# Optimization experiments

Measured on AMD Instinct MI355X. Metric: run time of the kernel, lower is better.

The kernel has to match this reference:

```python
import jax, jax.numpy as jnp
import numpy as np

PHI_C = 0.9
ALPHA = 0.9
EPS = 1e-06
K_MAX = 100


def setup_inputs() -> dict:
    key = jax.random.key(0)
    k1, k2, k3 = jax.random.split(key, 3)
    B, D_IN, D_H, D_OUT = 16384, 1024, 4096, 1024
    x = jax.random.normal(k1, (B, D_IN), dtype=jnp.float32)
    W1 = jax.random.normal(k2, (D_IN, D_H), dtype=jnp.float32) * 0.02
    b1 = jnp.zeros((D_H,), dtype=jnp.float32)
    W2 = jax.random.normal(k3, (D_H, D_OUT), dtype=jnp.float32) * 0.02
    b2 = jnp.zeros((D_OUT,), dtype=jnp.float32)
    return {"x": x, "W1": W1, "b1": b1, "W2": W2, "b2": b2}


def _base_net(x, W1, b1, W2, b2):
    h = jax.nn.relu(x @ W1 + b1)
    return h @ W2 + b2  # [B, D_OUT]


def _fixed_point(out):
    # y_{k+1} = y_k + alpha * phi_c * tanh(out - y_k), with early exit when
    # max|y_{k+1} - y_k| < eps (the converging step IS applied, as in torch).
    y0 = jnp.zeros_like(out)

    def step(carry, _):
        y, done = carry
        y_next = y + ALPHA * PHI_C * jnp.tanh(out - y)
        converged = jnp.max(jnp.abs(y_next - y)) < EPS
        y_new = jnp.where(done, y, y_next)
        return (y_new, done | converged), None

    (y, _), _ = jax.lax.scan(step, (y0, jnp.array(False)), None, length=K_MAX)
    return y


def reference(x, W1, b1, W2, b2):
    out = _base_net(x, W1, b1, W2, b2)
    return _fixed_point(out)
```

## Files before the change

kernel.cpp:

```cpp
#include <hip/hip_runtime.h>
#include <hip/hip_bf16.h>
#include <stdint.h>


#define DEV __device__ __forceinline__

typedef short bf16x8 __attribute__((ext_vector_type(8)));
typedef float f32x16 __attribute__((ext_vector_type(16)));

typedef __attribute__((address_space(1))) const unsigned char* gptr1_t;
typedef __attribute__((address_space(3))) unsigned char* lptr3_t;

DEV void async_copy16(const void* g, void* l) {
  __builtin_amdgcn_global_load_lds((gptr1_t)g, (lptr3_t)l, 16, 0, 0);
}

DEV unsigned short f2bf(float f) {
  union { float f; unsigned u; } v; v.f = f;
  unsigned u = v.u + 0x7FFFu + ((v.u >> 16) & 1u);
  return (unsigned short)(u >> 16);
}

#define BAR()    __builtin_amdgcn_s_barrier()
#define VMW(n)   asm volatile("s_waitcnt vmcnt(" #n ")" ::: "memory")
#define SCHEDB() __builtin_amdgcn_sched_barrier(0)


__global__ void cvt_f32_bf16(const float4* __restrict__ in,
                             ushort4* __restrict__ out, int n4) {
  int i = blockIdx.x * blockDim.x + threadIdx.x;
  if (i >= n4) return;
  float4 v = in[i];
  ushort4 o;
  o.x = f2bf(v.x); o.y = f2bf(v.y); o.z = f2bf(v.z); o.w = f2bf(v.w);
  out[i] = o;
}

__global__ void transpose_f32_bf16(const float* __restrict__ in,
                                   unsigned short* __restrict__ out,
                                   int R, int C) {
  __shared__ float tile[32][33];
  int c0 = blockIdx.x * 32, r0 = blockIdx.y * 32;
  int tx = threadIdx.x, ty = threadIdx.y;
#pragma unroll
  for (int i = 0; i < 32; i += 8)
    tile[ty + i][tx] = in[(long)(r0 + ty + i) * C + (c0 + tx)];
  __syncthreads();
#pragma unroll
  for (int i = 0; i < 32; i += 8)
    out[(long)(c0 + ty + i) * R + (r0 + tx)] = f2bf(tile[tx][ty + i]);
}


#define LDA(base, m, ks) \
  (*(const bf16x8*)((base) + abase + (m) * 4096 + (c0 ^ ((ks) << 5))))
#define LDB(base, n, ks) \
  (*(const bf16x8*)((base) + bbase + (n) * 4096 + (c0 ^ ((ks) << 5))))

#define COMPUTE(aB, bB)                                                       \
  _Pragma("unroll") for (int ks = 0; ks < 4; ++ks) {                          \
    bf16x8 af[4], bfr[4];                                                     \
    _Pragma("unroll") for (int i = 0; i < 4; ++i) {                           \
      af[i] = LDA(aB, i, ks);                                                 \
      bfr[i] = LDB(bB, i, ks);                                                \
    }                                                                         \
    _Pragma("unroll") for (int m_ = 0; m_ < 4; ++m_)                          \
    _Pragma("unroll") for (int n_ = 0; n_ < 4; ++n_)                          \
      acc[m_][n_] = __builtin_amdgcn_mfma_f32_32x32x16_bf16(                  \
          af[m_], bfr[n_], acc[m_][n_], 0, 0, 0);                             \
  }

#define STAGE(buf_, koff_)                                                    \
  _Pragma("unroll") for (int j = 0; j < 8; ++j) {                             \
    async_copy16(gAb + (size_t)j * 32 * K + (koff_),                          \
                 ldsAw + (buf_) * 32768 + j * 4096);                          \
    async_copy16(gBb + (size_t)j * 32 * K + (koff_),                          \
                 ldsBw + (buf_) * 32768 + j * 4096);                          \
  }

template <bool RELU_BF16>
__global__ __launch_bounds__(256, 1)
void gemm256(const unsigned short* __restrict__ A,
             const unsigned short* __restrict__ BT,
             const float* __restrict__ bias,
             void* __restrict__ Cout,
             int M, int N, int K, int nbn_shift) {
  extern __shared__ char lds[];
  char* ldsA = lds;
  char* ldsB = lds + 65536;

  const int tid = threadIdx.x;
  const int wave = tid >> 6, lane = tid & 63;
  const int wr = wave >> 1, wc = wave & 1;

  const int nwg = gridDim.x;
  const int wg = blockIdx.x;
  const int swz = (wg & 7) * (nwg >> 3) + (wg >> 3);
  const int bm = swz >> nbn_shift;
  const int bn = swz & ((1 << nbn_shift) - 1);
  const int m0 = bm << 8, n0 = bn << 8;

  const int srow = lane >> 3;
  const int skb = ((lane & 7) ^ srow) << 3;
  const unsigned short* gAb = A + (size_t)(m0 + wave * 8 + srow) * K + skb;
  const unsigned short* gBb = BT + (size_t)(n0 + wave * 8 + srow) * K + skb;
  char* ldsAw = ldsA + wave * 1024;
  char* ldsBw = ldsB + wave * 1024;

  const int cl31 = lane & 31, lg2 = lane >> 5;
  const int c0 = ((lg2 ^ (lane & 7)) << 4);
  const int abase = (wr * 128 + cl31) * 128;
  const int bbase = (wc * 128 + cl31) * 128;

  f32x16 acc[4][4] = {};

  STAGE(0, 0);
  STAGE(1, 64);
  VMW(16);
  BAR();

  const int NT = K >> 6;

  for (int t = 0; t < NT - 2; ++t) {
    const char* aB = ldsA + (t & 1) * 32768;
    const char* bB = ldsB + (t & 1) * 32768;
    COMPUTE(aB, bB);
    BAR();
    SCHEDB();
    STAGE(t & 1, (t + 2) << 6);
    VMW(16);
    BAR();
  }

  COMPUTE(ldsA, ldsB);
  BAR();
  VMW(0);
  BAR();
  COMPUTE((ldsA + 32768), (ldsB + 32768));

  const int ccol = n0 + wc * 128;
  const int crow = m0 + wr * 128;
  float bv[4];
#pragma unroll
  for (int n = 0; n < 4; ++n) bv[n] = bias[ccol + n * 32 + cl31];

  if (RELU_BF16) {
    unsigned short* O = (unsigned short*)Cout;
#pragma unroll
    for (int m = 0; m < 4; ++m)
#pragma unroll
      for (int rr = 0; rr < 4; ++rr)
#pragma unroll
        for (int q = 0; q < 4; ++q) {
          size_t r = (size_t)(crow + m * 32 + lg2 * 4 + q + 8 * rr) * N;
#pragma unroll
          for (int n = 0; n < 4; ++n) {
            float v = acc[m][n][rr * 4 + q] + bv[n];
            O[r + ccol + n * 32 + cl31] = f2bf(fmaxf(v, 0.0f));
          }
        }
  } else {
    float* O = (float*)Cout;
#pragma unroll
    for (int m = 0; m < 4; ++m)
#pragma unroll
      for (int rr = 0; rr < 4; ++rr)
#pragma unroll
        for (int q = 0; q < 4; ++q) {
          size_t r = (size_t)(crow + m * 32 + lg2 * 4 + q + 8 * rr) * N;
#pragma unroll
          for (int n = 0; n < 4; ++n)
            O[r + ccol + n * 32 + cl31] = acc[m][n][rr * 4 + q] + bv[n];
        }
  }
}


extern "C" void kernel_launch(void* const* d_in, const int* in_sizes, int n_in,
                              void* d_out, int out_size, void* d_ws,
                              size_t ws_size, hipStream_t stream) {
  const float* x  = (const float*)d_in[0];
  const float* W1 = (const float*)d_in[1];
  const float* b1 = (const float*)d_in[2];
  const float* W2 = (const float*)d_in[3];
  const float* b2 = (const float*)d_in[4];
  float* out = (float*)d_out;

  const int B = 16384, DIN = 1024, DH = 4096, DOUT = 1024;

  size_t need = (size_t)B * DIN * 2 + (size_t)DIN * DH * 2 +
                (size_t)DH * DOUT * 2 + (size_t)B * DH * 2;
  if (ws_size < need) return;

  char* ws = (char*)d_ws;
  unsigned short* xb  = (unsigned short*)ws;  ws += (size_t)B * DIN * 2;
  unsigned short* w1t = (unsigned short*)ws;  ws += (size_t)DIN * DH * 2;
  unsigned short* w2t = (unsigned short*)ws;  ws += (size_t)DH * DOUT * 2;
  unsigned short* h   = (unsigned short*)ws;

  hipFuncSetAttribute((const void*)gemm256<true>,
                      hipFuncAttributeMaxDynamicSharedMemorySize, 131072);
  hipFuncSetAttribute((const void*)gemm256<false>,
                      hipFuncAttributeMaxDynamicSharedMemorySize, 131072);

  int n4 = B * DIN / 4;
  cvt_f32_bf16<<<n4 / 256, 256, 0, stream>>>((const float4*)x, (ushort4*)xb, n4);
  transpose_f32_bf16<<<dim3(DH / 32, DIN / 32), dim3(32, 8), 0, stream>>>(W1, w1t, DIN, DH);
  transpose_f32_bf16<<<dim3(DOUT / 32, DH / 32), dim3(32, 8), 0, stream>>>(W2, w2t, DH, DOUT);

  gemm256<true><<<dim3((B / 256) * (DH / 256)), 256, 131072, stream>>>(
      xb, w1t, b1, h, B, DH, DIN, 4);
  gemm256<false><<<dim3((B / 256) * (DOUT / 256)), 256, 131072, stream>>>(
      h, w2t, b2, out, B, DOUT, DH, 2);
}
```

Measured before the change: 302.5 us.

## Make first GEMM persistent over four M-tiles and adjust LDS swizzle

The first GEMM now launches one block per CU, and each block walks four consecutive 256-row tiles for a fixed column tile. The double-buffered K pipeline runs continuously across tiles, with the bias/ReLU/bf16 epilogue inserted when each tile finishes. This is meant to remove per-block prologue/drain costs and wave-quantization tail effects. Both GEMMs also gain an extra wave-dependent XOR in the LDS swizzle to reduce bank conflicts. The epilogue stores now stall the pipeline mid-stream, and the grid mapping assumes the fixed problem shape.

After: 429.2 us. 1.42x slower.

```diff
diff --git a/kernel.cpp b/kernel.cpp
--- a/kernel.cpp
+++ b/kernel.cpp
@@ -52,17 +52,17 @@
 }
 
 
-#define LDA(base, m, ks) \
-  (*(const bf16x8*)((base) + abase + (m) * 4096 + (c0 ^ ((ks) << 5))))
-#define LDB(base, n, ks) \
-  (*(const bf16x8*)((base) + bbase + (n) * 4096 + (c0 ^ ((ks) << 5))))
-
-#define COMPUTE(aB, bB)                                                       \
+#define ILDA(base, m, ks) \
+  (*(const bf16x8*)((base) + i_abase + (m) * 4096 + (i_c0 ^ ((ks) << 5))))
+#define ILDB(base, n, ks) \
+  (*(const bf16x8*)((base) + i_bbase + (n) * 4096 + (i_c0 ^ ((ks) << 5))))
+
+#define ICOMPUTE(aB, bB)                                                      \
   _Pragma("unroll") for (int ks = 0; ks < 4; ++ks) {                          \
     bf16x8 af[4], bfr[4];                                                     \
     _Pragma("unroll") for (int i = 0; i < 4; ++i) {                           \
-      af[i] = LDA(aB, i, ks);                                                 \
-      bfr[i] = LDB(bB, i, ks);                                                \
+      af[i] = ILDA(aB, i, ks);                                                \
+      bfr[i] = ILDB(bB, i, ks);                                               \
     }                                                                         \
     _Pragma("unroll") for (int m_ = 0; m_ < 4; ++m_)                          \
     _Pragma("unroll") for (int n_ = 0; n_ < 4; ++n_)                          \
@@ -70,7 +70,103 @@
           af[m_], bfr[n_], acc[m_][n_], 0, 0, 0);                             \
   }
 
-#define STAGE(buf_, koff_)                                                    \
+
+#define PSTAGE(buf_, g_)                                                      \
+  { const int t_ = (g_) & 15;                                                 \
+    const size_t ja_ = (size_t)((g_) >> 4) * ((size_t)K << 8);                \
+    _Pragma("unroll") for (int j = 0; j < 8; ++j) {                           \
+      async_copy16(gAb + ja_ + (size_t)j * 32 * K + (t_ << 6),                \
+                   ldsAw + (buf_) * 32768 + j * 4096);                        \
+      async_copy16(gBb + (size_t)j * 32 * K + (t_ << 6),                      \
+                   ldsBw + (buf_) * 32768 + j * 4096);                        \
+    } }
+
+#define PEPI(j_)                                                              \
+  { const size_t crow = (size_t)m0base + (size_t)(j_) * 256 + wr * 128;       \
+    _Pragma("unroll") for (int m = 0; m < 4; ++m)                             \
+    _Pragma("unroll") for (int rr = 0; rr < 4; ++rr)                          \
+    _Pragma("unroll") for (int q = 0; q < 4; ++q) {                           \
+      size_t r = (crow + m * 32 + lg2 * 4 + q + 8 * rr) * Ndim;               \
+      _Pragma("unroll") for (int n = 0; n < 4; ++n) {                         \
+        float v = acc[m][n][rr * 4 + q] + bv[n];                              \
+        O[r + ccol + n * 32 + cl31] = f2bf(fmaxf(v, 0.0f));                   \
+      } } }
+
+#define ZEROACC()                                                             \
+  _Pragma("unroll") for (int m = 0; m < 4; ++m)                               \
+  _Pragma("unroll") for (int n = 0; n < 4; ++n)                               \
+  _Pragma("unroll") for (int e = 0; e < 16; ++e) acc[m][n][e] = 0.0f;
+
+__global__ __launch_bounds__(256, 1)
+void gemm_ilp4p(const unsigned short* __restrict__ A,
+                const unsigned short* __restrict__ BT,
+                const float* __restrict__ bias,
+                unsigned short* __restrict__ O,
+                int Kd, int Ndim) {
+  extern __shared__ char lds[];
+  char* ldsA = lds;
+  char* ldsB = lds + 65536;
+  const int K = Kd;
+
+  const int tid = threadIdx.x;
+  const int wave = tid >> 6, lane = tid & 63;
+  const int wr = wave >> 1, wc = wave & 1;
+
+  const int nwg = gridDim.x;
+  const int wg = blockIdx.x;
+  const int swz = (wg & 7) * (nwg >> 3) + (wg >> 3);
+  const int bn = swz & 15;
+  const int grp = swz >> 4;
+  const int n0 = bn << 8;
+  const int m0base = grp << 10;
+
+  const int srow = lane >> 3;
+  const int skb = (((lane & 7) ^ srow ^ wave) << 3);
+  const unsigned short* gAb = A + (size_t)(m0base + wave * 8 + srow) * K + skb;
+  const unsigned short* gBb = BT + (size_t)(n0 + wave * 8 + srow) * K + skb;
+  char* ldsAw = ldsA + wave * 1024;
+  char* ldsBw = ldsB + wave * 1024;
+
+  const int cl31 = lane & 31, lg2 = lane >> 5;
+  const int i_c0 = ((lg2 ^ (lane & 7) ^ ((lane >> 3) & 3)) << 4);
+  const int i_abase = (wr * 128 + cl31) * 128;
+  const int i_bbase = (wc * 128 + cl31) * 128;
+  const int ccol = n0 + wc * 128;
+
+  f32x16 acc[4][4] = {};
+  float bv[4];
+#pragma unroll
+  for (int n = 0; n < 4; ++n) bv[n] = bias[ccol + n * 32 + cl31];
+
+  PSTAGE(0, 0);
+  PSTAGE(1, 1);
+  VMW(16);
+  BAR();
+
+  for (int g = 0; g < 62; ++g) {
+    const char* aB = ldsA + (g & 1) * 32768;
+    const char* bB = ldsB + (g & 1) * 32768;
+    ICOMPUTE(aB, bB);
+    BAR();
+    if ((g & 15) == 15) {
+      PEPI(g >> 4);
+      ZEROACC();
+    }
+    SCHEDB();
+    PSTAGE(g & 1, g + 2);
+    VMW(16);
+    BAR();
+  }
+  ICOMPUTE(ldsA, ldsB);
+  BAR();
+  VMW(0);
+  BAR();
+  ICOMPUTE((ldsA + 32768), (ldsB + 32768));
+  PEPI(3);
+}
+
+
+#define ISTAGE(buf_, koff_)                                                   \
   _Pragma("unroll") for (int j = 0; j < 8; ++j) {                             \
     async_copy16(gAb + (size_t)j * 32 * K + (koff_),                          \
                  ldsAw + (buf_) * 32768 + j * 4096);                          \
@@ -80,11 +176,11 @@
 
 template <bool RELU_BF16>
 __global__ __launch_bounds__(256, 1)
-void gemm256(const unsigned short* __restrict__ A,
-             const unsigned short* __restrict__ BT,
-             const float* __restrict__ bias,
-             void* __restrict__ Cout,
-             int M, int N, int K, int nbn_shift) {
+void gemm_ilp4(const unsigned short* __restrict__ A,
+               const unsigned short* __restrict__ BT,
+               const float* __restrict__ bias,
+               void* __restrict__ Cout,
+               int M, int N, int K, int nbn_shift) {
   extern __shared__ char lds[];
   char* ldsA = lds;
   char* ldsB = lds + 65536;
@@ -101,21 +197,21 @@
   const int m0 = bm << 8, n0 = bn << 8;
 
   const int srow = lane >> 3;
-  const int skb = ((lane & 7) ^ srow) << 3;
+  const int skb = (((lane & 7) ^ srow ^ wave) << 3);
   const unsigned short* gAb = A + (size_t)(m0 + wave * 8 + srow) * K + skb;
   const unsigned short* gBb = BT + (size_t)(n0 + wave * 8 + srow) * K + skb;
   char* ldsAw = ldsA + wave * 1024;
   char* ldsBw = ldsB + wave * 1024;
 
   const int cl31 = lane & 31, lg2 = lane >> 5;
-  const int c0 = ((lg2 ^ (lane & 7)) << 4);
-  const int abase = (wr * 128 + cl31) * 128;
-  const int bbase = (wc * 128 + cl31) * 128;
+  const int i_c0 = ((lg2 ^ (lane & 7) ^ ((lane >> 3) & 3)) << 4);
+  const int i_abase = (wr * 128 + cl31) * 128;
+  const int i_bbase = (wc * 128 + cl31) * 128;
 
   f32x16 acc[4][4] = {};
 
-  STAGE(0, 0);
-  STAGE(1, 64);
+  ISTAGE(0, 0);
+  ISTAGE(1, 64);
   VMW(16);
   BAR();
 
@@ -124,19 +220,18 @@
   for (int t = 0; t < NT - 2; ++t) {
     const char* aB = ldsA + (t & 1) * 32768;
     const char* bB = ldsB + (t & 1) * 32768;
-    COMPUTE(aB, bB);
+    ICOMPUTE(aB, bB);
     BAR();
     SCHEDB();
-    STAGE(t & 1, (t + 2) << 6);
+    ISTAGE(t & 1, (t + 2) << 6);
     VMW(16);
     BAR();
   }
-
-  COMPUTE(ldsA, ldsB);
+  ICOMPUTE(ldsA, ldsB);
   BAR();
   VMW(0);
   BAR();
-  COMPUTE((ldsA + 32768), (ldsB + 32768));
+  ICOMPUTE((ldsA + 32768), (ldsB + 32768));
 
   const int ccol = n0 + wc * 128;
   const int crow = m0 + wr * 128;
@@ -198,9 +293,9 @@
   unsigned short* w2t = (unsigned short*)ws;  ws += (size_t)DH * DOUT * 2;
   unsigned short* h   = (unsigned short*)ws;
 
-  hipFuncSetAttribute((const void*)gemm256<true>,
+  hipFuncSetAttribute((const void*)gemm_ilp4p,
                       hipFuncAttributeMaxDynamicSharedMemorySize, 131072);
-  hipFuncSetAttribute((const void*)gemm256<false>,
+  hipFuncSetAttribute((const void*)gemm_ilp4<false>,
                       hipFuncAttributeMaxDynamicSharedMemorySize, 131072);
 
   int n4 = B * DIN / 4;
@@ -208,8 +303,7 @@
   transpose_f32_bf16<<<dim3(DH / 32, DIN / 32), dim3(32, 8), 0, stream>>>(W1, w1t, DIN, DH);
   transpose_f32_bf16<<<dim3(DOUT / 32, DH / 32), dim3(32, 8), 0, stream>>>(W2, w2t, DH, DOUT);
 
-  gemm256<true><<<dim3((B / 256) * (DH / 256)), 256, 131072, stream>>>(
-      xb, w1t, b1, h, B, DH, DIN, 4);
-  gemm256<false><<<dim3((B / 256) * (DOUT / 256)), 256, 131072, stream>>>(
+  gemm_ilp4p<<<dim3(256), 256, 131072, stream>>>(xb, w1t, b1, h, DIN, DH);
+  gemm_ilp4<false><<<dim3((B / 256) * (DOUT / 256)), 256, 131072, stream>>>(
       h, w2t, b2, out, B, DOUT, DH, 2);
 }
```
